# Kernel tuning notes

Measured on AMD Instinct MI355X. Metric: run time of the kernel, lower is better.

## Reference

```python
import jax, jax.numpy as jnp
import numpy as np

# (u, v) frequency bands, taken mod 8 as in the torch module
FREQ_BANDS = np.array([[0, 1], [1, 0], [1, 1], [2, 2], [3, 3], [4, 4]]) % 8


def setup_inputs() -> dict:
    key = jax.random.key(0)
    x = jax.random.normal(key, (64, 3, 512, 512), dtype=jnp.float32)
    return {"x": x}


def reference(x):
    B, C, H, W = x.shape
    gh, gw = H // 8, W // 8
    # unfold(2,8,8).unfold(3,8,8) -> [B, C, gh, gw, 8, 8]
    patches = x.reshape(B, C, gh, 8, gw, 8).transpose(0, 1, 2, 4, 3, 5)
    # 2D FFT over each 8x8 block, magnitude
    dct = jnp.abs(jnp.fft.fft2(patches))  # [B, C, gh, gw, 8, 8]
    # freq_mask only keeps the bins we index below, so masking is a no-op
    # for the gathered bins; gather all bands at once (vectorized over bands)
    u = jnp.asarray(FREQ_BANDS[:, 0])
    v = jnp.asarray(FREQ_BANDS[:, 1])
    band = dct[..., u, v]                 # [B, C, gh, gw, n_bands]
    feats = band.mean(axis=(2, 3))        # [B, C, n_bands]
    return feats.reshape(B, -1)           # [B, C * n_bands]
```

## Files before the change

### kernel.cpp

```cpp
#include <hip/hip_runtime.h>
#include <math.h>


#define IMG_W 512
#define IMG_PIX (512 * 512)

__global__ __launch_bounds__(256) void dct_band_kernel(const float* __restrict__ x,
                                                       float* __restrict__ out) {
    const int t    = threadIdx.x;
    const int lane = t & 63;
    const int wave = t >> 6;
    const int w    = blockIdx.x * 4 + wave;
    const int img  = w >> 7;
    const int bR   = (w >> 1) & 63;
    const int half = w & 1;

    const float* p = x + (size_t)img * IMG_PIX
                       + (size_t)(bR * 8) * IMG_W + half * 256 + lane * 4;

    float4 row[8];
#pragma unroll
    for (int r = 0; r < 8; ++r)
        row[r] = *(const float4*)(p + (size_t)r * IMG_W);

    const float C1 = 0.70710678118654752440f;
    const float ct[8] = {1.f,  C1, 0.f, -C1, -1.f, -C1, 0.f,  C1};
    const float st[8] = {0.f,  C1, 1.f,  C1,  0.f, -C1, -1.f, -C1};

    float F01r = 0.f, F01i = 0.f;
    float F10r = 0.f, F10i = 0.f;
    float F11r = 0.f, F11i = 0.f;
    float F22r = 0.f, F22i = 0.f;
    float F33r = 0.f, F33i = 0.f;
    float F44  = 0.f;

#pragma unroll
    for (int k = 0; k < 4; ++k) {
        const float x0 = (&row[0].x)[k];
        const float x1 = (&row[1].x)[k];
        const float x2 = (&row[2].x)[k];
        const float x3 = (&row[3].x)[k];
        const float x4 = (&row[4].x)[k];
        const float x5 = (&row[5].x)[k];
        const float x6 = (&row[6].x)[k];
        const float x7 = (&row[7].x)[k];

        const float h0  = x0 + x1 + x2 + x3 + x4 + x5 + x6 + x7;
        const float h1r = x0 - x4 + C1 * (x1 - x3 - x5 + x7);
        const float h1i = -(C1 * (x1 + x3 - x5 - x7) + x2 - x6);
        const float h2r = x0 - x2 + x4 - x6;
        const float h2i = -(x1 - x3 + x5 - x7);
        const float h3r = x0 - x4 + C1 * (-x1 + x3 + x5 - x7);
        const float h3i = -(C1 * (x1 + x3 - x5 - x7) - x2 + x6);
        const float h4  = x0 - x1 + x2 - x3 + x4 - x5 + x6 - x7;

        const float c1 = ct[k],           s1 = st[k];
        const float c2 = ct[(2 * k) & 7], s2 = st[(2 * k) & 7];
        const float c3 = ct[(3 * k) & 7], s3 = st[(3 * k) & 7];
        const float w4 = (k & 1) ? -1.f : 1.f;

        F01r += h0 * c1;               F01i -= h0 * s1;
        F10r += h1r;                   F10i += h1i;
        F11r += h1r * c1 + h1i * s1;   F11i += h1i * c1 - h1r * s1;
        F22r += h2r * c2 + h2i * s2;   F22i += h2i * c2 - h2r * s2;
        F33r += h3r * c3 + h3i * s3;   F33i += h3i * c3 - h3r * s3;
        F44  += h4 * w4;
    }

    const float sgn = (lane & 1) ? -1.f : 1.f;
    F01r *= sgn; F01i *= sgn;
    F11r *= sgn; F11i *= sgn;
    F33r *= sgn; F33i *= sgn;

    F01r += __shfl_xor(F01r, 1); F01i += __shfl_xor(F01i, 1);
    F10r += __shfl_xor(F10r, 1); F10i += __shfl_xor(F10i, 1);
    F11r += __shfl_xor(F11r, 1); F11i += __shfl_xor(F11i, 1);
    F22r += __shfl_xor(F22r, 1); F22i += __shfl_xor(F22i, 1);
    F33r += __shfl_xor(F33r, 1); F33i += __shfl_xor(F33i, 1);
    F44  += __shfl_xor(F44, 1);

    float m[6];
    m[0] = sqrtf(F01r * F01r + F01i * F01i);
    m[1] = sqrtf(F10r * F10r + F10i * F10i);
    m[2] = sqrtf(F11r * F11r + F11i * F11i);
    m[3] = sqrtf(F22r * F22r + F22i * F22i);
    m[4] = sqrtf(F33r * F33r + F33i * F33i);
    m[5] = fabsf(F44);

#pragma unroll
    for (int off = 32; off > 0; off >>= 1) {
#pragma unroll
        for (int k = 0; k < 6; ++k) m[k] += __shfl_down(m[k], off);
    }

    __shared__ float red[4][6];
    if (lane == 0) {
#pragma unroll
        for (int k = 0; k < 6; ++k) red[wave][k] = m[k];
    }
    __syncthreads();

    if (t < 6) {
        const float s = red[0][t] + red[1][t] + red[2][t] + red[3][t];
        atomicAdd(&out[img * 6 + t], s * (1.0f / 8192.0f));
    }
}

extern "C" void kernel_launch(void* const* d_in, const int* in_sizes, int n_in,
                              void* d_out, int out_size, void* d_ws, size_t ws_size,
                              hipStream_t stream) {
    const float* x = (const float*)d_in[0];
    float* out = (float*)d_out;

    hipMemsetAsync(d_out, 0, (size_t)out_size * sizeof(float), stream);

    dim3 grid(6144);
    dim3 block(256);
    dct_band_kernel<<<grid, block, 0, stream>>>(x, out);
}
```

Before: 270.5 us.

## Assign one full 8x8 block per lane and use nontemporal loads

New measurement: 276.5 us. 2.2% more time.

```diff
diff --git a/kernel.cpp b/kernel.cpp
--- a/kernel.cpp
+++ b/kernel.cpp
@@ -5,23 +5,26 @@
 #define IMG_W 512
 #define IMG_PIX (512 * 512)
 
+typedef float f4 __attribute__((ext_vector_type(4)));
+
 __global__ __launch_bounds__(256) void dct_band_kernel(const float* __restrict__ x,
                                                        float* __restrict__ out) {
     const int t    = threadIdx.x;
     const int lane = t & 63;
     const int wave = t >> 6;
     const int w    = blockIdx.x * 4 + wave;
-    const int img  = w >> 7;
-    const int bR   = (w >> 1) & 63;
-    const int half = w & 1;
+    const int img  = w >> 6;
+    const int bR   = w & 63;
 
     const float* p = x + (size_t)img * IMG_PIX
-                       + (size_t)(bR * 8) * IMG_W + half * 256 + lane * 4;
+                       + (size_t)(bR * 8) * IMG_W + lane * 8;
 
-    float4 row[8];
+    f4 rowlo[8], rowhi[8];
 #pragma unroll
-    for (int r = 0; r < 8; ++r)
-        row[r] = *(const float4*)(p + (size_t)r * IMG_W);
+    for (int r = 0; r < 8; ++r) {
+        rowlo[r] = __builtin_nontemporal_load((const f4*)(p + (size_t)r * IMG_W));
+        rowhi[r] = __builtin_nontemporal_load((const f4*)(p + (size_t)r * IMG_W + 4));
+    }
 
     const float C1 = 0.70710678118654752440f;
     const float ct[8] = {1.f,  C1, 0.f, -C1, -1.f, -C1, 0.f,  C1};
@@ -35,15 +38,17 @@
     float F44  = 0.f;
 
 #pragma unroll
-    for (int k = 0; k < 4; ++k) {
-        const float x0 = (&row[0].x)[k];
-        const float x1 = (&row[1].x)[k];
-        const float x2 = (&row[2].x)[k];
-        const float x3 = (&row[3].x)[k];
-        const float x4 = (&row[4].x)[k];
-        const float x5 = (&row[5].x)[k];
-        const float x6 = (&row[6].x)[k];
-        const float x7 = (&row[7].x)[k];
+    for (int c = 0; c < 8; ++c) {
+        const int  ci = c & 3;
+        const bool hi = c >= 4;
+        const float x0 = hi ? rowhi[0][ci] : rowlo[0][ci];
+        const float x1 = hi ? rowhi[1][ci] : rowlo[1][ci];
+        const float x2 = hi ? rowhi[2][ci] : rowlo[2][ci];
+        const float x3 = hi ? rowhi[3][ci] : rowlo[3][ci];
+        const float x4 = hi ? rowhi[4][ci] : rowlo[4][ci];
+        const float x5 = hi ? rowhi[5][ci] : rowlo[5][ci];
+        const float x6 = hi ? rowhi[6][ci] : rowlo[6][ci];
+        const float x7 = hi ? rowhi[7][ci] : rowlo[7][ci];
 
         const float h0  = x0 + x1 + x2 + x3 + x4 + x5 + x6 + x7;
         const float h1r = x0 - x4 + C1 * (x1 - x3 - x5 + x7);
@@ -54,10 +59,10 @@
         const float h3i = -(C1 * (x1 + x3 - x5 - x7) - x2 + x6);
         const float h4  = x0 - x1 + x2 - x3 + x4 - x5 + x6 - x7;
 
-        const float c1 = ct[k],           s1 = st[k];
-        const float c2 = ct[(2 * k) & 7], s2 = st[(2 * k) & 7];
-        const float c3 = ct[(3 * k) & 7], s3 = st[(3 * k) & 7];
-        const float w4 = (k & 1) ? -1.f : 1.f;
+        const float c1 = ct[c],           s1 = st[c];
+        const float c2 = ct[(2 * c) & 7], s2 = st[(2 * c) & 7];
+        const float c3 = ct[(3 * c) & 7], s3 = st[(3 * c) & 7];
+        const float w4 = (c & 1) ? -1.f : 1.f;
 
         F01r += h0 * c1;               F01i -= h0 * s1;
         F10r += h1r;                   F10i += h1i;
@@ -66,18 +71,6 @@
         F33r += h3r * c3 + h3i * s3;   F33i += h3i * c3 - h3r * s3;
         F44  += h4 * w4;
     }
-
-    const float sgn = (lane & 1) ? -1.f : 1.f;
-    F01r *= sgn; F01i *= sgn;
-    F11r *= sgn; F11i *= sgn;
-    F33r *= sgn; F33i *= sgn;
-
-    F01r += __shfl_xor(F01r, 1); F01i += __shfl_xor(F01i, 1);
-    F10r += __shfl_xor(F10r, 1); F10i += __shfl_xor(F10i, 1);
-    F11r += __shfl_xor(F11r, 1); F11i += __shfl_xor(F11i, 1);
-    F22r += __shfl_xor(F22r, 1); F22i += __shfl_xor(F22i, 1);
-    F33r += __shfl_xor(F33r, 1); F33i += __shfl_xor(F33i, 1);
-    F44  += __shfl_xor(F44, 1);
 
     float m[6];
     m[0] = sqrtf(F01r * F01r + F01i * F01i);
@@ -102,7 +95,7 @@
 
     if (t < 6) {
         const float s = red[0][t] + red[1][t] + red[2][t] + red[3][t];
-        atomicAdd(&out[img * 6 + t], s * (1.0f / 8192.0f));
+        atomicAdd(&out[img * 6 + t], s * (1.0f / 4096.0f));
     }
 }
 
@@ -114,7 +107,7 @@
 
     hipMemsetAsync(d_out, 0, (size_t)out_size * sizeof(float), stream);
 
-    dim3 grid(6144);
+    dim3 grid(3072);
     dim3 block(256);
     dct_band_kernel<<<grid, block, 0, stream>>>(x, out);
 }
```
